# Performance work log

Measured on AMD Instinct MI355X. Metric: run time of the kernel, lower is better.

The kernel has to match this reference:

```python
import jax, jax.numpy as jnp
import numpy as np

B = 768
D = 128
NUM_CLASSES = 32
MARGIN = 1.0
EPS = 1e-12  # avoid sqrt(0) -> nan grad on the diagonal


def setup_inputs() -> dict:
    key = jax.random.key(0)
    k1, k2 = jax.random.split(key)
    embeddings = jax.random.normal(k1, (B, D), dtype=jnp.float32)
    labels = jax.random.randint(k2, (B,), 0, NUM_CLASSES, dtype=jnp.int32)
    return {"embeddings": embeddings, "labels": labels}


def _triplet_loss(embeddings, labels, margin):
    n = embeddings.shape[0]
    # pairwise euclidean distances (torch.cdist p=2)
    sq = jnp.sum(embeddings * embeddings, axis=1)
    d2 = sq[:, None] + sq[None, :] - 2.0 * (embeddings @ embeddings.T)
    d = jnp.sqrt(jnp.maximum(d2, EPS))  # [B, B]

    same = labels[:, None] == labels[None, :]
    eye = jnp.eye(n, dtype=bool)
    pos_mask = same & ~eye          # valid anchor-positive pairs
    neg_mask = ~same                # valid negatives per anchor
    neg_exists = neg_mask.any(axis=1)

    # hardest negative per anchor (argmin over negatives) -- fallback
    d_neg_only = jnp.where(neg_mask, d, jnp.inf)
    hardest = jnp.argmin(d_neg_only, axis=1)  # [B]

    # semi-hard mask[i, j, k]: k is negative of i and pd < d[i,k] < pd + margin
    pd = d[:, :, None]   # d[i, j]
    nd = d[:, None, :]   # d[i, k]
    semi = neg_mask[:, None, :] & (nd > pd) & (nd < pd + margin)  # [B,B,B] bool
    semi_any = semi.any(axis=2)                 # [B, B]
    first_semi = jnp.argmax(semi, axis=2)       # first True index, like negative_indices[mask][0]

    neg_idx = jnp.where(semi_any, first_semi, hardest[:, None])  # [B, B]
    neg_d = jnp.take_along_axis(d, neg_idx, axis=1)              # [B, B]

    valid = pos_mask & neg_exists[:, None]
    per_triplet = jax.nn.relu(d - neg_d + margin)  # relu(pos - neg + margin)
    cnt = jnp.sum(valid)
    loss = jnp.sum(jnp.where(valid, per_triplet, 0.0)) / jnp.maximum(cnt, 1).astype(per_triplet.dtype)
    return loss


def reference(embeddings, labels):
    return _triplet_loss(embeddings, labels, MARGIN)
```

## Files before the change

### kernel.cpp

```cpp
#include <hip/hip_runtime.h>
#include <math.h>

#define NB 768
#define ND 128
#define NC 12
#define APB 3
#define TL_MARGIN 1.0f
#define TL_EPS 1e-12f


__global__ __launch_bounds__(256) void transpose_sq_kernel(
    const float* __restrict__ E, float* __restrict__ ET, float* __restrict__ sq)
{
    __shared__ float part[4];
    const int b    = blockIdx.x;
    const int tid  = threadIdx.x;
    const int lane = tid & 63;
    const int wave = tid >> 6;

    const int idx = b * 256 + tid;
    const float v = E[idx];
    const int j = idx >> 7;
    const int k = idx & 127;
    ET[(size_t)k * NB + j] = v;

    float s = v * v;
    #pragma unroll
    for (int off = 32; off > 0; off >>= 1) s += __shfl_xor(s, off);
    if (lane == 0) part[wave] = s;
    __syncthreads();
    if (tid == 0) {
        sq[2 * b]     = part[0] + part[1];
        sq[2 * b + 1] = part[2] + part[3];
    }
}

__global__ __launch_bounds__(384) void triplet_fused_kernel(
    const float* __restrict__ E, const float* __restrict__ ET,
    const float* __restrict__ sq, const int* __restrict__ L,
    float* __restrict__ psum, float* __restrict__ pcnt)
{
    __shared__ float drow[APB][NB];

    const int tid  = threadIdx.x;
    const int lane = tid & 63;
    const int wave = tid >> 6;
    int i0 = blockIdx.x * APB;
    i0 = __builtin_amdgcn_readfirstlane(i0);

    const float* __restrict__ A0 = E + (size_t)(i0 + 0) * ND;
    const float* __restrict__ A1 = E + (size_t)(i0 + 1) * ND;
    const float* __restrict__ A2 = E + (size_t)(i0 + 2) * ND;
    const float sqa0 = sq[i0], sqa1 = sq[i0 + 1], sqa2 = sq[i0 + 2];

    const float2* __restrict__ Bp = (const float2*)ET + (wave * 64 + lane);
    float px0 = 0.f, py0 = 0.f, px1 = 0.f, py1 = 0.f, px2 = 0.f, py2 = 0.f;
    #pragma unroll 8
    for (int k = 0; k < ND; ++k) {
        float2 b = Bp[(size_t)k * 384];
        float a0 = A0[k], a1 = A1[k], a2 = A2[k];
        px0 += a0 * b.x; py0 += a0 * b.y;
        px1 += a1 * b.x; py1 += a1 * b.y;
        px2 += a2 * b.x; py2 += a2 * b.y;
    }
    const int j0 = wave * 128 + lane * 2;
    const float2 sj = *(const float2*)(sq + j0);
    {
        float2 d;
        d.x = sqrtf(fmaxf(sqa0 + sj.x - 2.f * px0, TL_EPS));
        d.y = sqrtf(fmaxf(sqa0 + sj.y - 2.f * py0, TL_EPS));
        *(float2*)&drow[0][j0] = d;
        d.x = sqrtf(fmaxf(sqa1 + sj.x - 2.f * px1, TL_EPS));
        d.y = sqrtf(fmaxf(sqa1 + sj.y - 2.f * py1, TL_EPS));
        *(float2*)&drow[1][j0] = d;
        d.x = sqrtf(fmaxf(sqa2 + sj.x - 2.f * px2, TL_EPS));
        d.y = sqrtf(fmaxf(sqa2 + sj.y - 2.f * py2, TL_EPS));
        *(float2*)&drow[2][j0] = d;
    }
    __syncthreads();

    if (wave < APB) {
        const int ia = i0 + wave;
        const int li = L[ia];
        unsigned negm = 0u, posm = 0u;
        float dk[NC];
        #pragma unroll
        for (int c = 0; c < NC; ++c) {
            int j = c * 64 + lane;
            dk[c] = drow[wave][j];
            int lj = L[j];
            if (lj != li)     negm |= (1u << c);
            else if (j != ia) posm |= (1u << c);
        }

        float bv = INFINITY;
        #pragma unroll
        for (int c = 0; c < NC; ++c)
            if ((negm >> c) & 1u) bv = fminf(bv, dk[c]);
        #pragma unroll
        for (int off = 32; off > 0; off >>= 1)
            bv = fminf(bv, __shfl_xor(bv, off));
        const float hval = bv;

        float lsum = 0.f, lcnt = 0.f;
        if (isfinite(hval)) {
            #pragma unroll
            for (int c = 0; c < NC; ++c) {
                unsigned long long pm = __ballot((posm >> c) & 1u);
                while (pm) {
                    const int sl = __builtin_ctzll(pm);
                    pm &= pm - 1;
                    const float pd = __shfl(dk[c], sl);
                    float nd = hval;
                    #pragma unroll
                    for (int c2 = 0; c2 < NC; ++c2) {
                        bool pred = ((negm >> c2) & 1u) &&
                                    (dk[c2] > pd) && (dk[c2] < pd + TL_MARGIN);
                        unsigned long long m = __ballot(pred);
                        if (m) { nd = __shfl(dk[c2], __builtin_ctzll(m)); break; }
                    }
                    lsum += fmaxf(pd - nd + TL_MARGIN, 0.f);
                    lcnt += 1.f;
                }
            }
        }
        if (lane == 0) { psum[ia] = lsum; pcnt[ia] = lcnt; }
    }
}

__global__ __launch_bounds__(64) void triplet_finalize_kernel(
    const float* __restrict__ psum, const float* __restrict__ pcnt,
    float* __restrict__ out)
{
    const int lane = threadIdx.x;
    float a = 0.f, b = 0.f;
    for (int j = lane; j < NB; j += 64) { a += psum[j]; b += pcnt[j]; }
    #pragma unroll
    for (int off = 32; off > 0; off >>= 1) {
        a += __shfl_xor(a, off);
        b += __shfl_xor(b, off);
    }
    if (lane == 0) out[0] = a / fmaxf(b, 1.f);
}

extern "C" void kernel_launch(void* const* d_in, const int* in_sizes, int n_in,
                              void* d_out, int out_size, void* d_ws, size_t ws_size,
                              hipStream_t stream) {
    const float* E = (const float*)d_in[0];
    const int*   L = (const int*)d_in[1];
    char* ws = (char*)d_ws;
    float* ET   = (float*)(ws);
    float* sq   = (float*)(ws + 0x60000);
    float* psum = (float*)(ws + 0x61000);
    float* pcnt = (float*)(ws + 0x61C00);
    float* out  = (float*)d_out;

    transpose_sq_kernel<<<NB * ND / 256, 256, 0, stream>>>(E, ET, sq);
    triplet_fused_kernel<<<NB / APB, 384, 0, stream>>>(E, ET, sq, L, psum, pcnt);
    triplet_finalize_kernel<<<1, 64, 0, stream>>>(psum, pcnt, out);
}
```

Baseline: 31.32 us.

## Fuse finalize into main kernel via fixed-point atomics and last-block ticket

Removes the separate finalize kernel launch by accumulating per-anchor sums into a 64-bit fixed-point atomic counter and having the last block, detected by an atomic ticket, compute the mean. Counters are zeroed in the first kernel. The distance phase now uses 768 threads with one column per thread instead of 384 threads handling float2 pairs, which raises parallelism but leaves most waves idle during the triplet phase. Fixed-point scaling adds small rounding and depends on sums staying within range.

New measurement: 43.44 us. 38.7% more time.

```diff
diff --git a/kernel.cpp b/kernel.cpp
--- a/kernel.cpp
+++ b/kernel.cpp
@@ -7,16 +7,21 @@
 #define APB 3
 #define TL_MARGIN 1.0f
 #define TL_EPS 1e-12f
+#define SCALE 16777216.0f
 
 
 __global__ __launch_bounds__(256) void transpose_sq_kernel(
-    const float* __restrict__ E, float* __restrict__ ET, float* __restrict__ sq)
+    const float* __restrict__ E, float* __restrict__ ET, float* __restrict__ sq,
+    unsigned long long* __restrict__ psumI, int* __restrict__ pcntI,
+    int* __restrict__ ticket)
 {
     __shared__ float part[4];
     const int b    = blockIdx.x;
     const int tid  = threadIdx.x;
     const int lane = tid & 63;
     const int wave = tid >> 6;
+
+    if (b == 0 && tid == 0) { *psumI = 0ull; *pcntI = 0; *ticket = 0; }
 
     const int idx = b * 256 + tid;
     const float v = E[idx];
@@ -35,10 +40,11 @@
     }
 }
 
-__global__ __launch_bounds__(384) void triplet_fused_kernel(
+__global__ __launch_bounds__(768) void triplet_fused_kernel(
     const float* __restrict__ E, const float* __restrict__ ET,
     const float* __restrict__ sq, const int* __restrict__ L,
-    float* __restrict__ psum, float* __restrict__ pcnt)
+    unsigned long long* __restrict__ psumI, int* __restrict__ pcntI,
+    int* __restrict__ ticket, float* __restrict__ out)
 {
     __shared__ float drow[APB][NB];
 
@@ -53,29 +59,20 @@
     const float* __restrict__ A2 = E + (size_t)(i0 + 2) * ND;
     const float sqa0 = sq[i0], sqa1 = sq[i0 + 1], sqa2 = sq[i0 + 2];
 
-    const float2* __restrict__ Bp = (const float2*)ET + (wave * 64 + lane);
-    float px0 = 0.f, py0 = 0.f, px1 = 0.f, py1 = 0.f, px2 = 0.f, py2 = 0.f;
-    #pragma unroll 8
-    for (int k = 0; k < ND; ++k) {
-        float2 b = Bp[(size_t)k * 384];
-        float a0 = A0[k], a1 = A1[k], a2 = A2[k];
-        px0 += a0 * b.x; py0 += a0 * b.y;
-        px1 += a1 * b.x; py1 += a1 * b.y;
-        px2 += a2 * b.x; py2 += a2 * b.y;
-    }
-    const int j0 = wave * 128 + lane * 2;
-    const float2 sj = *(const float2*)(sq + j0);
     {
-        float2 d;
-        d.x = sqrtf(fmaxf(sqa0 + sj.x - 2.f * px0, TL_EPS));
-        d.y = sqrtf(fmaxf(sqa0 + sj.y - 2.f * py0, TL_EPS));
-        *(float2*)&drow[0][j0] = d;
-        d.x = sqrtf(fmaxf(sqa1 + sj.x - 2.f * px1, TL_EPS));
-        d.y = sqrtf(fmaxf(sqa1 + sj.y - 2.f * py1, TL_EPS));
-        *(float2*)&drow[1][j0] = d;
-        d.x = sqrtf(fmaxf(sqa2 + sj.x - 2.f * px2, TL_EPS));
-        d.y = sqrtf(fmaxf(sqa2 + sj.y - 2.f * py2, TL_EPS));
-        *(float2*)&drow[2][j0] = d;
+        const float* __restrict__ Bcol = ET + (wave * 64 + lane);
+        float p0 = 0.f, p1 = 0.f, p2 = 0.f;
+        #pragma unroll 8
+        for (int k = 0; k < ND; ++k) {
+            float b = Bcol[(size_t)k * NB];
+            float a0 = A0[k], a1 = A1[k], a2 = A2[k];
+            p0 += a0 * b; p1 += a1 * b; p2 += a2 * b;
+        }
+        const int j = wave * 64 + lane;
+        const float sjv = sq[j];
+        drow[0][j] = sqrtf(fmaxf(sqa0 + sjv - 2.f * p0, TL_EPS));
+        drow[1][j] = sqrtf(fmaxf(sqa1 + sjv - 2.f * p1, TL_EPS));
+        drow[2][j] = sqrtf(fmaxf(sqa2 + sjv - 2.f * p2, TL_EPS));
     }
     __syncthreads();
 
@@ -124,23 +121,24 @@
                 }
             }
         }
-        if (lane == 0) { psum[ia] = lsum; pcnt[ia] = lcnt; }
+        if (lane == 0) {
+            atomicAdd(psumI, (unsigned long long)llrintf(lsum * SCALE));
+            atomicAdd(pcntI, (int)(lcnt + 0.5f));
+        }
     }
-}
+    __syncthreads();
 
-__global__ __launch_bounds__(64) void triplet_finalize_kernel(
-    const float* __restrict__ psum, const float* __restrict__ pcnt,
-    float* __restrict__ out)
-{
-    const int lane = threadIdx.x;
-    float a = 0.f, b = 0.f;
-    for (int j = lane; j < NB; j += 64) { a += psum[j]; b += pcnt[j]; }
-    #pragma unroll
-    for (int off = 32; off > 0; off >>= 1) {
-        a += __shfl_xor(a, off);
-        b += __shfl_xor(b, off);
+    if (tid == 0) {
+        __threadfence();
+        int t = atomicAdd(ticket, 1);
+        if (t == (int)gridDim.x - 1) {
+            unsigned long long s = atomicAdd(psumI, 0ull);
+            int c = atomicAdd(pcntI, 0);
+            double sum = (double)s * (1.0 / (double)SCALE);
+            int cd = c > 1 ? c : 1;
+            out[0] = (float)(sum / (double)cd);
+        }
     }
-    if (lane == 0) out[0] = a / fmaxf(b, 1.f);
 }
 
 extern "C" void kernel_launch(void* const* d_in, const int* in_sizes, int n_in,
@@ -151,11 +149,11 @@
     char* ws = (char*)d_ws;
     float* ET   = (float*)(ws);
     float* sq   = (float*)(ws + 0x60000);
-    float* psum = (float*)(ws + 0x61000);
-    float* pcnt = (float*)(ws + 0x61C00);
+    unsigned long long* psumI = (unsigned long long*)(ws + 0x61000);
+    int* pcntI  = (int*)(ws + 0x61008);
+    int* ticket = (int*)(ws + 0x6100C);
     float* out  = (float*)d_out;
 
-    transpose_sq_kernel<<<NB * ND / 256, 256, 0, stream>>>(E, ET, sq);
-    triplet_fused_kernel<<<NB / APB, 384, 0, stream>>>(E, ET, sq, L, psum, pcnt);
-    triplet_finalize_kernel<<<1, 64, 0, stream>>>(psum, pcnt, out);
+    transpose_sq_kernel<<<NB * ND / 256, 256, 0, stream>>>(E, ET, sq, psumI, pcntI, ticket);
+    triplet_fused_kernel<<<NB / APB, 768, 0, stream>>>(E, ET, sq, L, psumI, pcntI, ticket, out);
 }
```

## Merge three kernels into one cooperative kernel with grid-wide syncs

Applied to the files above, without the earlier changes.

Replaces the transpose/sq, fused triplet and finalize launches with a single cooperative kernel that uses grid.sync between phases. Row squared norms are now kept as per-wave partial sums and combined on read. The aim is to remove two kernel launch gaps. In exchange it adds two grid-wide barriers, relies on all 256 blocks being co-resident, and depends on the cooperative launch succeeding, since its return value is ignored.

Result: slower. 91.90 us (+193.5%).

```diff
diff --git a/kernel.cpp b/kernel.cpp
--- a/kernel.cpp
+++ b/kernel.cpp
@@ -1,80 +1,78 @@
 #include <hip/hip_runtime.h>
+#include <hip/hip_cooperative_groups.h>
 #include <math.h>
+
+namespace cg = cooperative_groups;
 
 #define NB 768
 #define ND 128
 #define NC 12
 #define APB 3
+#define NTH 384
 #define TL_MARGIN 1.0f
 #define TL_EPS 1e-12f
 
 
-__global__ __launch_bounds__(256) void transpose_sq_kernel(
-    const float* __restrict__ E, float* __restrict__ ET, float* __restrict__ sq)
-{
-    __shared__ float part[4];
-    const int b    = blockIdx.x;
-    const int tid  = threadIdx.x;
-    const int lane = tid & 63;
-    const int wave = tid >> 6;
-
-    const int idx = b * 256 + tid;
-    const float v = E[idx];
-    const int j = idx >> 7;
-    const int k = idx & 127;
-    ET[(size_t)k * NB + j] = v;
-
-    float s = v * v;
-    #pragma unroll
-    for (int off = 32; off > 0; off >>= 1) s += __shfl_xor(s, off);
-    if (lane == 0) part[wave] = s;
-    __syncthreads();
-    if (tid == 0) {
-        sq[2 * b]     = part[0] + part[1];
-        sq[2 * b + 1] = part[2] + part[3];
-    }
-}
-
-__global__ __launch_bounds__(384) void triplet_fused_kernel(
-    const float* __restrict__ E, const float* __restrict__ ET,
-    const float* __restrict__ sq, const int* __restrict__ L,
-    float* __restrict__ psum, float* __restrict__ pcnt)
+__global__ __launch_bounds__(NTH) void triplet_all_kernel(
+    const float* __restrict__ E, const int* __restrict__ L,
+    float* __restrict__ ET, float* __restrict__ sqp,
+    float* __restrict__ psum, float* __restrict__ pcnt,
+    float* __restrict__ out)
 {
     __shared__ float drow[APB][NB];
 
     const int tid  = threadIdx.x;
     const int lane = tid & 63;
     const int wave = tid >> 6;
-    int i0 = blockIdx.x * APB;
+    const int bid  = blockIdx.x;
+
+    {
+        const int gid = bid * NTH + tid;
+        const float v = E[gid];
+        const int j = gid >> 7;
+        const int k = gid & 127;
+        ET[(size_t)k * NB + j] = v;
+        float s = v * v;
+        #pragma unroll
+        for (int off = 32; off > 0; off >>= 1) s += __shfl_xor(s, off);
+        if (lane == 0) sqp[gid >> 6] = s;
+    }
+    cg::this_grid().sync();
+
+    int i0 = bid * APB;
     i0 = __builtin_amdgcn_readfirstlane(i0);
 
     const float* __restrict__ A0 = E + (size_t)(i0 + 0) * ND;
     const float* __restrict__ A1 = E + (size_t)(i0 + 1) * ND;
     const float* __restrict__ A2 = E + (size_t)(i0 + 2) * ND;
-    const float sqa0 = sq[i0], sqa1 = sq[i0 + 1], sqa2 = sq[i0 + 2];
+    const float sqa0 = sqp[2 * i0]     + sqp[2 * i0 + 1];
+    const float sqa1 = sqp[2 * i0 + 2] + sqp[2 * i0 + 3];
+    const float sqa2 = sqp[2 * i0 + 4] + sqp[2 * i0 + 5];
 
-    const float2* __restrict__ Bp = (const float2*)ET + (wave * 64 + lane);
-    float px0 = 0.f, py0 = 0.f, px1 = 0.f, py1 = 0.f, px2 = 0.f, py2 = 0.f;
-    #pragma unroll 8
-    for (int k = 0; k < ND; ++k) {
-        float2 b = Bp[(size_t)k * 384];
-        float a0 = A0[k], a1 = A1[k], a2 = A2[k];
-        px0 += a0 * b.x; py0 += a0 * b.y;
-        px1 += a1 * b.x; py1 += a1 * b.y;
-        px2 += a2 * b.x; py2 += a2 * b.y;
-    }
-    const int j0 = wave * 128 + lane * 2;
-    const float2 sj = *(const float2*)(sq + j0);
     {
+        const float2* __restrict__ Bp = (const float2*)ET + (wave * 64 + lane);
+        float px0 = 0.f, py0 = 0.f, px1 = 0.f, py1 = 0.f, px2 = 0.f, py2 = 0.f;
+        #pragma unroll 8
+        for (int k = 0; k < ND; ++k) {
+            float2 b = Bp[(size_t)k * 384];
+            float a0 = A0[k], a1 = A1[k], a2 = A2[k];
+            px0 += a0 * b.x; py0 += a0 * b.y;
+            px1 += a1 * b.x; py1 += a1 * b.y;
+            px2 += a2 * b.x; py2 += a2 * b.y;
+        }
+        const int j0 = wave * 128 + lane * 2;
+        const float4 sp = *(const float4*)(sqp + 2 * j0);
+        const float sjx = sp.x + sp.y;
+        const float sjy = sp.z + sp.w;
         float2 d;
-        d.x = sqrtf(fmaxf(sqa0 + sj.x - 2.f * px0, TL_EPS));
-        d.y = sqrtf(fmaxf(sqa0 + sj.y - 2.f * py0, TL_EPS));
+        d.x = sqrtf(fmaxf(sqa0 + sjx - 2.f * px0, TL_EPS));
+        d.y = sqrtf(fmaxf(sqa0 + sjy - 2.f * py0, TL_EPS));
         *(float2*)&drow[0][j0] = d;
-        d.x = sqrtf(fmaxf(sqa1 + sj.x - 2.f * px1, TL_EPS));
-        d.y = sqrtf(fmaxf(sqa1 + sj.y - 2.f * py1, TL_EPS));
+        d.x = sqrtf(fmaxf(sqa1 + sjx - 2.f * px1, TL_EPS));
+        d.y = sqrtf(fmaxf(sqa1 + sjy - 2.f * py1, TL_EPS));
         *(float2*)&drow[1][j0] = d;
-        d.x = sqrtf(fmaxf(sqa2 + sj.x - 2.f * px2, TL_EPS));
-        d.y = sqrtf(fmaxf(sqa2 + sj.y - 2.f * py2, TL_EPS));
+        d.x = sqrtf(fmaxf(sqa2 + sjx - 2.f * px2, TL_EPS));
+        d.y = sqrtf(fmaxf(sqa2 + sjy - 2.f * py2, TL_EPS));
         *(float2*)&drow[2][j0] = d;
     }
     __syncthreads();
@@ -126,21 +124,18 @@
         }
         if (lane == 0) { psum[ia] = lsum; pcnt[ia] = lcnt; }
     }
-}
+    cg::this_grid().sync();
 
-__global__ __launch_bounds__(64) void triplet_finalize_kernel(
-    const float* __restrict__ psum, const float* __restrict__ pcnt,
-    float* __restrict__ out)
-{
-    const int lane = threadIdx.x;
-    float a = 0.f, b = 0.f;
-    for (int j = lane; j < NB; j += 64) { a += psum[j]; b += pcnt[j]; }
-    #pragma unroll
-    for (int off = 32; off > 0; off >>= 1) {
-        a += __shfl_xor(a, off);
-        b += __shfl_xor(b, off);
+    if (bid == 0 && wave == 0) {
+        float a = 0.f, b = 0.f;
+        for (int j = lane; j < NB; j += 64) { a += psum[j]; b += pcnt[j]; }
+        #pragma unroll
+        for (int off = 32; off > 0; off >>= 1) {
+            a += __shfl_xor(a, off);
+            b += __shfl_xor(b, off);
+        }
+        if (lane == 0) out[0] = a / fmaxf(b, 1.f);
     }
-    if (lane == 0) out[0] = a / fmaxf(b, 1.f);
 }
 
 extern "C" void kernel_launch(void* const* d_in, const int* in_sizes, int n_in,
@@ -150,12 +145,13 @@
     const int*   L = (const int*)d_in[1];
     char* ws = (char*)d_ws;
     float* ET   = (float*)(ws);
-    float* sq   = (float*)(ws + 0x60000);
-    float* psum = (float*)(ws + 0x61000);
-    float* pcnt = (float*)(ws + 0x61C00);
+    float* sqp  = (float*)(ws + 0x60000);
+    float* psum = (float*)(ws + 0x61800);
+    float* pcnt = (float*)(ws + 0x62400);
     float* out  = (float*)d_out;
 
-    transpose_sq_kernel<<<NB * ND / 256, 256, 0, stream>>>(E, ET, sq);
-    triplet_fused_kernel<<<NB / APB, 384, 0, stream>>>(E, ET, sq, L, psum, pcnt);
-    triplet_finalize_kernel<<<1, 64, 0, stream>>>(psum, pcnt, out);
+    void* args[] = {(void*)&E, (void*)&L, (void*)&ET, (void*)&sqp,
+                    (void*)&psum, (void*)&pcnt, (void*)&out};
+    (void)hipLaunchCooperativeKernel((const void*)triplet_all_kernel,
+                                     dim3(NB / APB), dim3(NTH), args, 0, stream);
 }
```

## Compute twelve anchor rows per block with 768 threads, one column each

Applied to the files above, without the earlier changes.

Each block now handles 12 anchors instead of 3, using 768 threads where every thread computes one distance column for all 12 anchors. Each loaded ET element is therefore reused across 12 anchor rows, and all 12 waves take part in the semi-hard mining phase instead of only 3 of the 6. The cost is fewer blocks (64 instead of 256) on a GPU with many CUs, and more registers per thread for 12 accumulators.

Result: slower. 59.41 us (+89.7%).

```diff
diff --git a/kernel.cpp b/kernel.cpp
--- a/kernel.cpp
+++ b/kernel.cpp
@@ -4,7 +4,8 @@
 #define NB 768
 #define ND 128
 #define NC 12
-#define APB 3
+#define APB 12
+#define NTH 768
 #define TL_MARGIN 1.0f
 #define TL_EPS 1e-12f
 
@@ -35,7 +36,7 @@
     }
 }
 
-__global__ __launch_bounds__(384) void triplet_fused_kernel(
+__global__ __launch_bounds__(NTH) void triplet_fused_kernel(
     const float* __restrict__ E, const float* __restrict__ ET,
     const float* __restrict__ sq, const int* __restrict__ L,
     float* __restrict__ psum, float* __restrict__ pcnt)
@@ -48,38 +49,32 @@
     int i0 = blockIdx.x * APB;
     i0 = __builtin_amdgcn_readfirstlane(i0);
 
-    const float* __restrict__ A0 = E + (size_t)(i0 + 0) * ND;
-    const float* __restrict__ A1 = E + (size_t)(i0 + 1) * ND;
-    const float* __restrict__ A2 = E + (size_t)(i0 + 2) * ND;
-    const float sqa0 = sq[i0], sqa1 = sq[i0 + 1], sqa2 = sq[i0 + 2];
+    float sqa[APB];
+    #pragma unroll
+    for (int a = 0; a < APB; ++a) sqa[a] = sq[i0 + a];
 
-    const float2* __restrict__ Bp = (const float2*)ET + (wave * 64 + lane);
-    float px0 = 0.f, py0 = 0.f, px1 = 0.f, py1 = 0.f, px2 = 0.f, py2 = 0.f;
-    #pragma unroll 8
-    for (int k = 0; k < ND; ++k) {
-        float2 b = Bp[(size_t)k * 384];
-        float a0 = A0[k], a1 = A1[k], a2 = A2[k];
-        px0 += a0 * b.x; py0 += a0 * b.y;
-        px1 += a1 * b.x; py1 += a1 * b.y;
-        px2 += a2 * b.x; py2 += a2 * b.y;
-    }
-    const int j0 = wave * 128 + lane * 2;
-    const float2 sj = *(const float2*)(sq + j0);
     {
-        float2 d;
-        d.x = sqrtf(fmaxf(sqa0 + sj.x - 2.f * px0, TL_EPS));
-        d.y = sqrtf(fmaxf(sqa0 + sj.y - 2.f * py0, TL_EPS));
-        *(float2*)&drow[0][j0] = d;
-        d.x = sqrtf(fmaxf(sqa1 + sj.x - 2.f * px1, TL_EPS));
-        d.y = sqrtf(fmaxf(sqa1 + sj.y - 2.f * py1, TL_EPS));
-        *(float2*)&drow[1][j0] = d;
-        d.x = sqrtf(fmaxf(sqa2 + sj.x - 2.f * px2, TL_EPS));
-        d.y = sqrtf(fmaxf(sqa2 + sj.y - 2.f * py2, TL_EPS));
-        *(float2*)&drow[2][j0] = d;
+        const int j = wave * 64 + lane;
+        const float* __restrict__ Bcol = ET + j;
+        float p[APB];
+        #pragma unroll
+        for (int a = 0; a < APB; ++a) p[a] = 0.f;
+
+        #pragma unroll 16
+        for (int k = 0; k < ND; ++k) {
+            float b = Bcol[(size_t)k * NB];
+            #pragma unroll
+            for (int a = 0; a < APB; ++a)
+                p[a] += E[(size_t)(i0 + a) * ND + k] * b;
+        }
+        const float sjv = sq[j];
+        #pragma unroll
+        for (int a = 0; a < APB; ++a)
+            drow[a][j] = sqrtf(fmaxf(sqa[a] + sjv - 2.f * p[a], TL_EPS));
     }
     __syncthreads();
 
-    if (wave < APB) {
+    {
         const int ia = i0 + wave;
         const int li = L[ia];
         unsigned negm = 0u, posm = 0u;
@@ -156,6 +151,6 @@
     float* out  = (float*)d_out;
 
     transpose_sq_kernel<<<NB * ND / 256, 256, 0, stream>>>(E, ET, sq);
-    triplet_fused_kernel<<<NB / APB, 384, 0, stream>>>(E, ET, sq, L, psum, pcnt);
+    triplet_fused_kernel<<<NB / APB, NTH, 0, stream>>>(E, ET, sq, L, psum, pcnt);
     triplet_finalize_kernel<<<1, 64, 0, stream>>>(psum, pcnt, out);
 }
```
